# Kernel optimization log

Measured on AMD Instinct MI355X. Metric: run time of the kernel, lower is better.

The kernel has to match this reference:

```python
import jax, jax.numpy as jnp
import numpy as np

M, N, K, D_IN = 200, 6, 25, 784
GAMMA, EPS = 0.5, 0.5
TOTAL = M * N


def setup_inputs() -> dict:
    key = jax.random.key(0)
    ks = jax.random.split(key, 8)
    B = 16384
    def lin(kk, shape, fan_in):
        bound = 1.0 / np.sqrt(fan_in)
        return jax.random.uniform(kk, shape, jnp.float32, -bound, bound)
    return {
        "batch_x": jax.random.normal(ks[0], (B, D_IN), jnp.float32),
        "Wa": lin(ks[1], (M, D_IN), D_IN),
        "ba": lin(ks[2], (M,), D_IN),
        "Wb": lin(ks[3], (TOTAL, TOTAL), TOTAL),
        "bb": lin(ks[4], (TOTAL,), TOTAL),
        "Wd": lin(ks[5], (D_IN, M), M),
        "bd": lin(ks[6], (D_IN,), M),
    }


def _step(params, carry, x):
    Wa, ba, Wb, bb, Wd, bd = params
    x_b, phi, psi = carry
    # sigma: per-group drive broadcast over cells + full recurrent term, shape (m, n)
    z_a = (Wa @ x + ba)[:, None]                      # (m, 1)
    z_b = (Wb @ x_b + bb).reshape(M, N)               # (m, n)
    sigma = z_a + z_b
    # inhibited activity
    pi = (1.0 - phi) * (sigma - sigma.min() + 1.0)    # (m, n)
    lambda_i = pi.max(axis=1)                         # (m,)
    # top-1 cell per group (scatter of topk indices == one-hot argmax)
    M_pi = jax.nn.one_hot(jnp.argmax(pi, axis=1), N, dtype=sigma.dtype)
    # top-k groups
    _, idx = jax.lax.top_k(lambda_i, K)
    M_lambda = jnp.zeros((M,), sigma.dtype).at[idx].set(1.0)[:, None]
    y = jnp.tanh(M_pi * M_lambda * sigma)             # (m, n)
    x_a_pred = Wd @ y.max(axis=1) + bd                # (D_in,)
    # memory / inhibition updates
    psi_n = jnp.maximum(EPS * psi, y)
    phi_n = jnp.maximum(GAMMA * phi, y)
    alpha = psi_n.sum()
    alpha = jnp.where(alpha == 0.0, 1.0, alpha)
    x_b_n = (psi_n / alpha).reshape(-1)
    # original detaches the recurrent state each step
    carry_n = (jax.lax.stop_gradient(x_b_n),
               jax.lax.stop_gradient(phi_n),
               jax.lax.stop_gradient(psi_n))
    return carry_n, x_a_pred


def reference(batch_x, Wa, ba, Wb, bb, Wd, bd):
    params = (Wa, ba, Wb, bb, Wd, bd)
    carry0 = (jnp.zeros((TOTAL,), batch_x.dtype),
              jnp.zeros((M, N), batch_x.dtype),
              jnp.zeros((M, N), batch_x.dtype))
    (x_b, phi, psi), preds = jax.lax.scan(
        lambda c, x: _step(params, c, x), carry0, batch_x)
    return preds, x_b, phi, psi
```

## Files before the change

kernel.cpp:

```cpp
#include <hip/hip_runtime.h>
#include <math.h>

#define Tn   16384
#define Mg   200
#define Nc   6
#define TOT  1200
#define Kk   25
#define Din  784
#define PADG 8
#define CST  (Mg * PADG)

__global__ void transpose_k(const float* __restrict__ src, float* __restrict__ dst,
                            int R, int C) {
    __shared__ float tile[32][33];
    int bx = blockIdx.x * 32, by = blockIdx.y * 32;
    int x = bx + threadIdx.x;
    for (int j = 0; j < 32; j += 8) {
        int y = by + threadIdx.y + j;
        if (x < C && y < R) tile[threadIdx.y + j][threadIdx.x] = src[(size_t)y * C + x];
    }
    __syncthreads();
    int x2 = by + threadIdx.x;
    for (int j = 0; j < 32; j += 8) {
        int y2 = bx + threadIdx.y + j;
        if (x2 < R && y2 < C) dst[(size_t)y2 * R + x2] = tile[threadIdx.x][threadIdx.y + j];
    }
}

__global__ void wbT_pad_k(const float* __restrict__ Wb, float* __restrict__ WbTp) {
    __shared__ float tile[32][33];
    int e0 = blockIdx.x * 32, i0 = blockIdx.y * 32;
    for (int j = 0; j < 32; j += 8) {
        int i = i0 + threadIdx.y + j, e = e0 + threadIdx.x;
        if (i < TOT && e < TOT) tile[threadIdx.y + j][threadIdx.x] = Wb[(size_t)i * TOT + e];
    }
    __syncthreads();
    for (int j = 0; j < 32; j += 8) {
        int e = e0 + threadIdx.y + j, i = i0 + threadIdx.x;
        if (i < TOT && e < TOT) {
            int g = i / 6, c = i - 6 * g;
            WbTp[(size_t)e * CST + PADG * g + c] = tile[threadIdx.x][threadIdx.y + j];
        }
    }
}

__global__ void za_k(const float* __restrict__ X, const float* __restrict__ Wa,
                     const float* __restrict__ ba, float* __restrict__ Za) {
    __shared__ float xs[16][788];
    const int tid = threadIdx.x;
    const int t0  = blockIdx.x * 16;
    for (int idx = tid; idx < 16 * Din; idx += 256) {
        int tt = idx / Din, kk = idx - tt * Din;
        xs[tt][kk] = X[(size_t)(t0 + tt) * Din + kk];
    }
    __syncthreads();
    const int tq = tid & 15, gq = tid >> 4;
    const float4* xrow = reinterpret_cast<const float4*>(&xs[tq][0]);
    for (int g = gq; g < Mg; g += 16) {
        float acc = ba[g];
        const float4* wrow = reinterpret_cast<const float4*>(Wa + (size_t)g * Din);
        for (int k4 = 0; k4 < Din / 4; ++k4) {
            float4 a = xrow[k4], b = wrow[k4];
            acc = fmaf(a.x, b.x, acc); acc = fmaf(a.y, b.y, acc);
            acc = fmaf(a.z, b.z, acc); acc = fmaf(a.w, b.w, acc);
        }
        Za[(size_t)(t0 + tq) * Mg + g] = acc;
    }
}

__launch_bounds__(256, 1)
__global__ void serial_k(const float* __restrict__ Za, const float* __restrict__ WbTp,
                         const float* __restrict__ bb,
                         float* __restrict__ Yval, int* __restrict__ Yidx,
                         float* __restrict__ outTail) {
    __shared__ alignas(16) unsigned long long lamk[Mg];
    __shared__ alignas(16) unsigned long long sel[26];
    __shared__ alignas(16) float red[4];

    const int tid = threadIdx.x;
    const bool own = (tid < Mg);
    const int b = Nc * tid;

    float u0=0.f,u1=0.f,u2=0.f,u3=0.f,u4=0.f,u5=0.f;
    float p0=0.f,p1=0.f,p2=0.f,p3=0.f,p4=0.f,p5=0.f;
    float b0=0.f,b1=0.f,b2=0.f,b3=0.f,b4=0.f,b5=0.f;
    float alpha = 0.f;
    float zb = 0.f;
    if (own) {
        b0=bb[b]; b1=bb[b+1]; b2=bb[b+2]; b3=bb[b+3]; b4=bb[b+4]; b5=bb[b+5];
        zb = Za[tid];
    }
    if (tid == 255) sel[25] = 0ull;
    __syncthreads();

    const float* basep = WbTp + PADG * tid;

    for (int t = 0; t < Tn; ++t) {
        float inv = (alpha == 0.f) ? 1.f : (1.f / alpha);
        float s0=0,s1=0,s2=0,s3=0,s4=0,s5=0;
        float lmin = INFINITY;
        if (own) {
            float c = zb;
            s0 = fmaf(u0, inv, b0 + c); s1 = fmaf(u1, inv, b1 + c);
            s2 = fmaf(u2, inv, b2 + c); s3 = fmaf(u3, inv, b3 + c);
            s4 = fmaf(u4, inv, b4 + c); s5 = fmaf(u5, inv, b5 + c);
            lmin = fminf(fminf(fminf(s0,s1),fminf(s2,s3)),fminf(s4,s5));
        }
        for (int o = 32; o; o >>= 1) lmin = fminf(lmin, __shfl_down(lmin, o));
        if ((tid & 63) == 0) red[tid >> 6] = lmin;
        __syncthreads();

        float zn = 0.f;
        if (own && t + 1 < Tn) zn = Za[(size_t)(t + 1) * Mg + tid];

        unsigned long long myk = 0ull;
        float sb = 0.f, pb = 0.f;
        int bj = 0;
        if (own) {
            float4 r4 = *reinterpret_cast<const float4*>(red);
            float m1 = 1.f - fminf(fminf(r4.x, r4.y), fminf(r4.z, r4.w));
            float best = -INFINITY;
            float sa[6] = {s0,s1,s2,s3,s4,s5};
            float pa[6] = {p0,p1,p2,p3,p4,p5};
            #pragma unroll
            for (int j = 0; j < Nc; ++j) {
                float pv = (1.f - pa[j]) * (sa[j] + m1);
                if (pv > best) { best = pv; bj = j; sb = sa[j]; pb = pa[j]; }
            }
            unsigned int ub = __float_as_uint(best);
            ub ^= (unsigned int)(((int)ub) >> 31) | 0x80000000u;
            myk = ((unsigned long long)ub << 32) | (unsigned long long)(0xFFFFFFFFu - (unsigned)tid);
            lamk[tid] = myk;
        }
        __syncthreads();

        float d = 0.f;
        if (own) {
            float y  = tanhf(sb);
            float yv = fmaxf(y, 0.f);
            float dc = fmaxf(y - 0.5f * pb, 0.f);
            int r = 0;
            const ulonglong2* L = reinterpret_cast<const ulonglong2*>(lamk);
            #pragma unroll
            for (int q = 0; q < Mg / 2; ++q) {
                ulonglong2 kv = L[q];
                r += (kv.x > myk) + (kv.y > myk);
            }
            if (r < Kk) {
                d = dc;
                unsigned off = (unsigned)((b + bj) * CST);
                sel[r] = ((unsigned long long)off << 32) |
                         (unsigned long long)__float_as_uint(d);
                Yval[(size_t)t * Kk + r] = yv;
                Yidx[(size_t)t * Kk + r] = tid;
            }
            p0 = 0.5f*p0 + ((bj==0)?d:0.f); p1 = 0.5f*p1 + ((bj==1)?d:0.f);
            p2 = 0.5f*p2 + ((bj==2)?d:0.f); p3 = 0.5f*p3 + ((bj==3)?d:0.f);
            p4 = 0.5f*p4 + ((bj==4)?d:0.f); p5 = 0.5f*p5 + ((bj==5)?d:0.f);
        }
        __syncthreads();

        if (own) {
            ulonglong2 sraw[13];
            const ulonglong2* S = reinterpret_cast<const ulonglong2*>(sel);
            #pragma unroll
            for (int q = 0; q < 13; ++q) sraw[q] = S[q];
            float sd[Kk]; int so[Kk];
            #pragma unroll
            for (int k = 0; k < Kk; ++k) {
                unsigned long long v = (k & 1) ? sraw[k >> 1].y : sraw[k >> 1].x;
                sd[k] = __uint_as_float((unsigned)v);
                so[k] = (int)(v >> 32);
            }
            float asum = 0.f;
            #pragma unroll
            for (int k = 0; k < Kk; ++k) asum += sd[k];
            alpha = 0.5f * alpha + asum;

            float4 va[Kk]; float2 vb[Kk];
            #pragma unroll
            for (int k = 0; k < Kk; ++k) {
                const float* c = basep + so[k];
                va[k] = *reinterpret_cast<const float4*>(c);
                vb[k] = *reinterpret_cast<const float2*>(c + 4);
            }
            float a0=0.5f*u0, a1=0.5f*u1, a2=0.5f*u2, a3=0.5f*u3, a4=0.5f*u4, a5=0.5f*u5;
            #pragma unroll
            for (int k = 0; k < Kk; ++k) {
                float dk = sd[k];
                a0 = fmaf(dk, va[k].x, a0); a1 = fmaf(dk, va[k].y, a1);
                a2 = fmaf(dk, va[k].z, a2); a3 = fmaf(dk, va[k].w, a3);
                a4 = fmaf(dk, vb[k].x, a4); a5 = fmaf(dk, vb[k].y, a5);
            }
            u0=a0; u1=a1; u2=a2; u3=a3; u4=a4; u5=a5;
            zb = zn;
        }
    }

    if (own) {
        float inv = (alpha == 0.f) ? 1.f : (1.f / alpha);
        float pa[6] = {p0,p1,p2,p3,p4,p5};
        #pragma unroll
        for (int j = 0; j < Nc; ++j) {
            outTail[b + j]           = pa[j] * inv;
            outTail[TOT + b + j]     = pa[j];
            outTail[2 * TOT + b + j] = pa[j];
        }
    }
}

__global__ void preds_k(const float* __restrict__ Yval, const int* __restrict__ Yidx,
                        const float* __restrict__ WdT, const float* __restrict__ bd,
                        float* __restrict__ out) {
    const int t = blockIdx.x;
    __shared__ float sv[Kk];
    __shared__ int   si[Kk];
    if (threadIdx.x < Kk) {
        sv[threadIdx.x] = Yval[(size_t)t * Kk + threadIdx.x];
        si[threadIdx.x] = Yidx[(size_t)t * Kk + threadIdx.x];
    }
    __syncthreads();
    for (int d = threadIdx.x; d < Din; d += 256) {
        float acc = bd[d];
        #pragma unroll
        for (int k = 0; k < Kk; ++k)
            acc = fmaf(sv[k], WdT[(size_t)si[k] * Din + d], acc);
        out[(size_t)t * Din + d] = acc;
    }
}

extern "C" void kernel_launch(void* const* d_in, const int* in_sizes, int n_in,
                              void* d_out, int out_size, void* d_ws, size_t ws_size,
                              hipStream_t stream) {
    const float* X  = (const float*)d_in[0];
    const float* Wa = (const float*)d_in[1];
    const float* ba = (const float*)d_in[2];
    const float* Wb = (const float*)d_in[3];
    const float* bb = (const float*)d_in[4];
    const float* Wd = (const float*)d_in[5];
    const float* bd = (const float*)d_in[6];
    float* out = (float*)d_out;

    float* w    = (float*)d_ws;
    float* Za   = w;
    float* WbTp = Za   + (size_t)Tn * Mg;
    float* WdT  = WbTp + (size_t)TOT * CST;
    float* Yv   = WdT  + (size_t)Mg * Din;
    int*   Yi   = (int*)(Yv + (size_t)Tn * Kk);

    dim3 tb(32, 8);
    wbT_pad_k<<<dim3(38, 38), tb, 0, stream>>>(Wb, WbTp);
    transpose_k<<<dim3((Mg + 31) / 32, (Din + 31) / 32), tb, 0, stream>>>(Wd, WdT, Din, Mg);
    za_k<<<Tn / 16, 256, 0, stream>>>(X, Wa, ba, Za);
    serial_k<<<1, 256, 0, stream>>>(Za, WbTp, bb, Yv, Yi, out + (size_t)Tn * Din);
    preds_k<<<Tn, 256, 0, stream>>>(Yv, Yi, WdT, bd, out);
}
```

Measured before the change: 82.81 ms.

## Split serial recurrence across two thread halves with shared partial sums

Doubles the serial kernel to 512 threads. Each half computes part of the top-k rank count, and each half gathers about half of the 25 selected Wb columns. The second half's partial recurrent contribution goes through shared memory and is added at the start of the next step. The padded Wb transpose is replaced by a plain transpose read as float2 pairs, and an extra barrier per step is added. The aim is to shorten the per-step latency chain, at the cost of more synchronisation.

```diff
diff --git a/kernel.cpp b/kernel.cpp
--- a/kernel.cpp
+++ b/kernel.cpp
@@ -7,8 +7,6 @@
 #define TOT  1200
 #define Kk   25
 #define Din  784
-#define PADG 8
-#define CST  (Mg * PADG)
 
 __global__ void transpose_k(const float* __restrict__ src, float* __restrict__ dst,
                             int R, int C) {
@@ -24,23 +22,6 @@
     for (int j = 0; j < 32; j += 8) {
         int y2 = bx + threadIdx.y + j;
         if (x2 < R && y2 < C) dst[(size_t)y2 * R + x2] = tile[threadIdx.x][threadIdx.y + j];
-    }
-}
-
-__global__ void wbT_pad_k(const float* __restrict__ Wb, float* __restrict__ WbTp) {
-    __shared__ float tile[32][33];
-    int e0 = blockIdx.x * 32, i0 = blockIdx.y * 32;
-    for (int j = 0; j < 32; j += 8) {
-        int i = i0 + threadIdx.y + j, e = e0 + threadIdx.x;
-        if (i < TOT && e < TOT) tile[threadIdx.y + j][threadIdx.x] = Wb[(size_t)i * TOT + e];
-    }
-    __syncthreads();
-    for (int j = 0; j < 32; j += 8) {
-        int e = e0 + threadIdx.y + j, i = i0 + threadIdx.x;
-        if (i < TOT && e < TOT) {
-            int g = i / 6, c = i - 6 * g;
-            WbTp[(size_t)e * CST + PADG * g + c] = tile[threadIdx.x][threadIdx.y + j];
-        }
     }
 }
 
@@ -68,55 +49,62 @@
     }
 }
 
-__launch_bounds__(256, 1)
-__global__ void serial_k(const float* __restrict__ Za, const float* __restrict__ WbTp,
+__launch_bounds__(512, 1)
+__global__ void serial_k(const float* __restrict__ Za, const float* __restrict__ WbT,
                          const float* __restrict__ bb,
                          float* __restrict__ Yval, int* __restrict__ Yidx,
                          float* __restrict__ outTail) {
     __shared__ alignas(16) unsigned long long lamk[Mg];
     __shared__ alignas(16) unsigned long long sel[26];
     __shared__ alignas(16) float red[4];
+    __shared__ alignas(16) float uB[TOT];
+    __shared__ int rpart[Mg];
 
     const int tid = threadIdx.x;
-    const bool own = (tid < Mg);
-    const int b = Nc * tid;
+    const bool Aside = (tid < 256);
+    const int g = Aside ? tid : tid - 256;
+    const bool own  = (g < Mg);
+    const bool ownA = Aside && own;
+    const int b = Nc * g;
 
     float u0=0.f,u1=0.f,u2=0.f,u3=0.f,u4=0.f,u5=0.f;
     float p0=0.f,p1=0.f,p2=0.f,p3=0.f,p4=0.f,p5=0.f;
     float b0=0.f,b1=0.f,b2=0.f,b3=0.f,b4=0.f,b5=0.f;
-    float alpha = 0.f;
-    float zb = 0.f;
-    if (own) {
+    float alpha = 0.f, zb = 0.f;
+    if (ownA) {
         b0=bb[b]; b1=bb[b+1]; b2=bb[b+2]; b3=bb[b+3]; b4=bb[b+4]; b5=bb[b+5];
-        zb = Za[tid];
-    }
-    if (tid == 255) sel[25] = 0ull;
-    __syncthreads();
-
-    const float* basep = WbTp + PADG * tid;
+        zb = Za[g];
+    }
+    for (int i = tid; i < TOT; i += 512) uB[i] = 0.f;
+    __syncthreads();
+
+    const float* baseW = WbT + b;
 
     for (int t = 0; t < Tn; ++t) {
-        float inv = (alpha == 0.f) ? 1.f : (1.f / alpha);
+        float zn = 0.f;
+        if (ownA && t + 1 < Tn) zn = Za[(size_t)(t + 1) * Mg + g];
+
+        unsigned long long myk = 0ull;
+        float sb=0.f, pb=0.f; int bj = 0;
+        float lmin = INFINITY;
         float s0=0,s1=0,s2=0,s3=0,s4=0,s5=0;
-        float lmin = INFINITY;
-        if (own) {
-            float c = zb;
-            s0 = fmaf(u0, inv, b0 + c); s1 = fmaf(u1, inv, b1 + c);
-            s2 = fmaf(u2, inv, b2 + c); s3 = fmaf(u3, inv, b3 + c);
-            s4 = fmaf(u4, inv, b4 + c); s5 = fmaf(u5, inv, b5 + c);
+        if (ownA) {
+            const float2* q = reinterpret_cast<const float2*>(&uB[b]);
+            float2 q0=q[0], q1=q[1], q2=q[2];
+            u0+=q0.x; u1+=q0.y; u2+=q1.x; u3+=q1.y; u4+=q2.x; u5+=q2.y;
+            float inv = (alpha == 0.f) ? 1.f : (1.f / alpha);
+            s0 = fmaf(u0, inv, b0 + zb); s1 = fmaf(u1, inv, b1 + zb);
+            s2 = fmaf(u2, inv, b2 + zb); s3 = fmaf(u3, inv, b3 + zb);
+            s4 = fmaf(u4, inv, b4 + zb); s5 = fmaf(u5, inv, b5 + zb);
             lmin = fminf(fminf(fminf(s0,s1),fminf(s2,s3)),fminf(s4,s5));
         }
-        for (int o = 32; o; o >>= 1) lmin = fminf(lmin, __shfl_down(lmin, o));
-        if ((tid & 63) == 0) red[tid >> 6] = lmin;
-        __syncthreads();
-
-        float zn = 0.f;
-        if (own && t + 1 < Tn) zn = Za[(size_t)(t + 1) * Mg + tid];
-
-        unsigned long long myk = 0ull;
-        float sb = 0.f, pb = 0.f;
-        int bj = 0;
-        if (own) {
+        if (Aside) {
+            for (int o = 32; o; o >>= 1) lmin = fminf(lmin, __shfl_down(lmin, o));
+            if ((tid & 63) == 0) red[tid >> 6] = lmin;
+        }
+        __syncthreads();
+
+        if (ownA) {
             float4 r4 = *reinterpret_cast<const float4*>(red);
             float m1 = 1.f - fminf(fminf(r4.x, r4.y), fminf(r4.z, r4.w));
             float best = -INFINITY;
@@ -127,32 +115,36 @@
                 float pv = (1.f - pa[j]) * (sa[j] + m1);
                 if (pv > best) { best = pv; bj = j; sb = sa[j]; pb = pa[j]; }
             }
-            unsigned int ub = __float_as_uint(best);
-            ub ^= (unsigned int)(((int)ub) >> 31) | 0x80000000u;
-            myk = ((unsigned long long)ub << 32) | (unsigned long long)(0xFFFFFFFFu - (unsigned)tid);
-            lamk[tid] = myk;
-        }
-        __syncthreads();
-
-        float d = 0.f;
+            unsigned ub = __float_as_uint(best);
+            ub ^= (unsigned)(((int)ub) >> 31) | 0x80000000u;
+            myk = ((unsigned long long)ub << 32) | (unsigned long long)(0xFFFFFFFFu - (unsigned)g);
+            lamk[g] = myk;
+        }
+        __syncthreads();
+
+        int rr = 0; float yv = 0.f, dc = 0.f;
         if (own) {
-            float y  = tanhf(sb);
-            float yv = fmaxf(y, 0.f);
-            float dc = fmaxf(y - 0.5f * pb, 0.f);
-            int r = 0;
-            const ulonglong2* L = reinterpret_cast<const ulonglong2*>(lamk);
-            #pragma unroll
-            for (int q = 0; q < Mg / 2; ++q) {
+            if (!Aside) myk = lamk[g];
+            const ulonglong2* L = reinterpret_cast<const ulonglong2*>(lamk) + (Aside ? 0 : 50);
+            #pragma unroll
+            for (int q = 0; q < 50; ++q) {
                 ulonglong2 kv = L[q];
-                r += (kv.x > myk) + (kv.y > myk);
-            }
+                rr += (kv.x > myk) + (kv.y > myk);
+            }
+            if (ownA) { float y = tanhf(sb); yv = fmaxf(y, 0.f); dc = fmaxf(y - 0.5f * pb, 0.f); }
+        }
+        if (!Aside && own) rpart[g] = rr;
+        __syncthreads();
+
+        if (ownA) {
+            int r = rr + rpart[g];
+            float d = 0.f;
             if (r < Kk) {
                 d = dc;
-                unsigned off = (unsigned)((b + bj) * CST);
-                sel[r] = ((unsigned long long)off << 32) |
+                sel[r] = ((unsigned long long)(unsigned)((b + bj) * TOT) << 32) |
                          (unsigned long long)__float_as_uint(d);
                 Yval[(size_t)t * Kk + r] = yv;
-                Yidx[(size_t)t * Kk + r] = tid;
+                Yidx[(size_t)t * Kk + r] = g;
             }
             p0 = 0.5f*p0 + ((bj==0)?d:0.f); p1 = 0.5f*p1 + ((bj==1)?d:0.f);
             p2 = 0.5f*p2 + ((bj==2)?d:0.f); p3 = 0.5f*p3 + ((bj==3)?d:0.f);
@@ -172,32 +164,58 @@
                 sd[k] = __uint_as_float((unsigned)v);
                 so[k] = (int)(v >> 32);
             }
-            float asum = 0.f;
-            #pragma unroll
-            for (int k = 0; k < Kk; ++k) asum += sd[k];
-            alpha = 0.5f * alpha + asum;
-
-            float4 va[Kk]; float2 vb[Kk];
-            #pragma unroll
-            for (int k = 0; k < Kk; ++k) {
-                const float* c = basep + so[k];
-                va[k] = *reinterpret_cast<const float4*>(c);
-                vb[k] = *reinterpret_cast<const float2*>(c + 4);
-            }
-            float a0=0.5f*u0, a1=0.5f*u1, a2=0.5f*u2, a3=0.5f*u3, a4=0.5f*u4, a5=0.5f*u5;
-            #pragma unroll
-            for (int k = 0; k < Kk; ++k) {
-                float dk = sd[k];
-                a0 = fmaf(dk, va[k].x, a0); a1 = fmaf(dk, va[k].y, a1);
-                a2 = fmaf(dk, va[k].z, a2); a3 = fmaf(dk, va[k].w, a3);
-                a4 = fmaf(dk, vb[k].x, a4); a5 = fmaf(dk, vb[k].y, a5);
-            }
-            u0=a0; u1=a1; u2=a2; u3=a3; u4=a4; u5=a5;
-            zb = zn;
-        }
-    }
-
-    if (own) {
+            if (Aside) {
+                float asum = 0.f;
+                #pragma unroll
+                for (int k = 0; k < Kk; ++k) asum += sd[k];
+                alpha = 0.5f * alpha + asum;
+                float2 c0[13], c1[13], c2[13];
+                #pragma unroll
+                for (int k = 0; k < 13; ++k) {
+                    const float* cp = baseW + so[k];
+                    c0[k] = *reinterpret_cast<const float2*>(cp);
+                    c1[k] = *reinterpret_cast<const float2*>(cp + 2);
+                    c2[k] = *reinterpret_cast<const float2*>(cp + 4);
+                }
+                __builtin_amdgcn_sched_barrier(0);
+                float a0=0.5f*u0, a1=0.5f*u1, a2=0.5f*u2, a3=0.5f*u3, a4=0.5f*u4, a5=0.5f*u5;
+                #pragma unroll
+                for (int k = 0; k < 13; ++k) {
+                    float dk = sd[k];
+                    a0 = fmaf(dk, c0[k].x, a0); a1 = fmaf(dk, c0[k].y, a1);
+                    a2 = fmaf(dk, c1[k].x, a2); a3 = fmaf(dk, c1[k].y, a3);
+                    a4 = fmaf(dk, c2[k].x, a4); a5 = fmaf(dk, c2[k].y, a5);
+                }
+                u0=a0; u1=a1; u2=a2; u3=a3; u4=a4; u5=a5;
+                zb = zn;
+            } else {
+                float2 c0[12], c1[12], c2[12];
+                #pragma unroll
+                for (int k = 0; k < 12; ++k) {
+                    const float* cp = baseW + so[13 + k];
+                    c0[k] = *reinterpret_cast<const float2*>(cp);
+                    c1[k] = *reinterpret_cast<const float2*>(cp + 2);
+                    c2[k] = *reinterpret_cast<const float2*>(cp + 4);
+                }
+                __builtin_amdgcn_sched_barrier(0);
+                float a0=0,a1=0,a2=0,a3=0,a4=0,a5=0;
+                #pragma unroll
+                for (int k = 0; k < 12; ++k) {
+                    float dk = sd[13 + k];
+                    a0 = fmaf(dk, c0[k].x, a0); a1 = fmaf(dk, c0[k].y, a1);
+                    a2 = fmaf(dk, c1[k].x, a2); a3 = fmaf(dk, c1[k].y, a3);
+                    a4 = fmaf(dk, c2[k].x, a4); a5 = fmaf(dk, c2[k].y, a5);
+                }
+                float2* w = reinterpret_cast<float2*>(&uB[b]);
+                w[0] = make_float2(a0, a1);
+                w[1] = make_float2(a2, a3);
+                w[2] = make_float2(a4, a5);
+            }
+        }
+        __syncthreads();
+    }
+
+    if (ownA) {
         float inv = (alpha == 0.f) ? 1.f : (1.f / alpha);
         float pa[6] = {p0,p1,p2,p3,p4,p5};
         #pragma unroll
@@ -243,15 +261,15 @@
 
     float* w    = (float*)d_ws;
     float* Za   = w;
-    float* WbTp = Za   + (size_t)Tn * Mg;
-    float* WdT  = WbTp + (size_t)TOT * CST;
-    float* Yv   = WdT  + (size_t)Mg * Din;
+    float* WbT  = Za  + (size_t)Tn * Mg;
+    float* WdT  = WbT + (size_t)TOT * TOT;
+    float* Yv   = WdT + (size_t)Mg * Din;
     int*   Yi   = (int*)(Yv + (size_t)Tn * Kk);
 
     dim3 tb(32, 8);
-    wbT_pad_k<<<dim3(38, 38), tb, 0, stream>>>(Wb, WbTp);
+    transpose_k<<<dim3((TOT + 31) / 32, (TOT + 31) / 32), tb, 0, stream>>>(Wb, WbT, TOT, TOT);
     transpose_k<<<dim3((Mg + 31) / 32, (Din + 31) / 32), tb, 0, stream>>>(Wd, WdT, Din, Mg);
     za_k<<<Tn / 16, 256, 0, stream>>>(X, Wa, ba, Za);
-    serial_k<<<1, 256, 0, stream>>>(Za, WbTp, bb, Yv, Yi, out + (size_t)Tn * Din);
+    serial_k<<<1, 512, 0, stream>>>(Za, WbT, bb, Yv, Yi, out + (size_t)Tn * Din);
     preds_k<<<Tn, 256, 0, stream>>>(Yv, Yi, WdT, bd, out);
 }
```

Result: slower. 85.88 ms (+3.7%).

## Stage Za chunks in LDS and batch top-k outputs in serial kernel

Applied to the files above, without the earlier changes.

The serial kernel now copies 32 timesteps of Za into shared memory at a time instead of doing a per-step global load. It also buffers the packed (index, value) top-k outputs in LDS and writes them out once per chunk as 64-bit words. The Wb layout drops the padded 8-stride in favour of a plain transpose, so each gathered column now takes three float2 loads instead of a float4 plus a float2. A sched_barrier separates the loads from the FMAs. This is meant to take global-memory latency off the serial critical path, at the cost of a block sync every 32 steps and more LDS use.

```diff
diff --git a/kernel.cpp b/kernel.cpp
--- a/kernel.cpp
+++ b/kernel.cpp
@@ -7,8 +7,7 @@
 #define TOT  1200
 #define Kk   25
 #define Din  784
-#define PADG 8
-#define CST  (Mg * PADG)
+#define CH   32
 
 __global__ void transpose_k(const float* __restrict__ src, float* __restrict__ dst,
                             int R, int C) {
@@ -24,23 +23,6 @@
     for (int j = 0; j < 32; j += 8) {
         int y2 = bx + threadIdx.y + j;
         if (x2 < R && y2 < C) dst[(size_t)y2 * R + x2] = tile[threadIdx.x][threadIdx.y + j];
-    }
-}
-
-__global__ void wbT_pad_k(const float* __restrict__ Wb, float* __restrict__ WbTp) {
-    __shared__ float tile[32][33];
-    int e0 = blockIdx.x * 32, i0 = blockIdx.y * 32;
-    for (int j = 0; j < 32; j += 8) {
-        int i = i0 + threadIdx.y + j, e = e0 + threadIdx.x;
-        if (i < TOT && e < TOT) tile[threadIdx.y + j][threadIdx.x] = Wb[(size_t)i * TOT + e];
-    }
-    __syncthreads();
-    for (int j = 0; j < 32; j += 8) {
-        int e = e0 + threadIdx.y + j, i = i0 + threadIdx.x;
-        if (i < TOT && e < TOT) {
-            int g = i / 6, c = i - 6 * g;
-            WbTp[(size_t)e * CST + PADG * g + c] = tile[threadIdx.x][threadIdx.y + j];
-        }
     }
 }
 
@@ -69,13 +51,15 @@
 }
 
 __launch_bounds__(256, 1)
-__global__ void serial_k(const float* __restrict__ Za, const float* __restrict__ WbTp,
+__global__ void serial_k(const float* __restrict__ Za, const float* __restrict__ WbT,
                          const float* __restrict__ bb,
-                         float* __restrict__ Yval, int* __restrict__ Yidx,
+                         unsigned long long* __restrict__ YP,
                          float* __restrict__ outTail) {
     __shared__ alignas(16) unsigned long long lamk[Mg];
     __shared__ alignas(16) unsigned long long sel[26];
     __shared__ alignas(16) float red[4];
+    __shared__ alignas(16) float zs[CH * Mg];
+    __shared__ alignas(16) unsigned long long ypk[CH * Kk];
 
     const int tid = threadIdx.x;
     const bool own = (tid < Mg);
@@ -85,37 +69,40 @@
     float p0=0.f,p1=0.f,p2=0.f,p3=0.f,p4=0.f,p5=0.f;
     float b0=0.f,b1=0.f,b2=0.f,b3=0.f,b4=0.f,b5=0.f;
     float alpha = 0.f;
-    float zb = 0.f;
     if (own) {
         b0=bb[b]; b1=bb[b+1]; b2=bb[b+2]; b3=bb[b+3]; b4=bb[b+4]; b5=bb[b+5];
-        zb = Za[tid];
-    }
-    if (tid == 255) sel[25] = 0ull;
-    __syncthreads();
-
-    const float* basep = WbTp + PADG * tid;
+    }
+    #pragma unroll
+    for (int i = 0; i < 7; ++i) {
+        int idx = i * 1024 + tid * 4;
+        if (idx < CH * Mg) {
+            float4 v = *reinterpret_cast<const float4*>(Za + idx);
+            *reinterpret_cast<float4*>(zs + idx) = v;
+        }
+    }
+    __syncthreads();
+
+    const float* baseW = WbT + b;
 
     for (int t = 0; t < Tn; ++t) {
-        float inv = (alpha == 0.f) ? 1.f : (1.f / alpha);
+        const int tc = t & (CH - 1);
+
         float s0=0,s1=0,s2=0,s3=0,s4=0,s5=0;
         float lmin = INFINITY;
         if (own) {
-            float c = zb;
-            s0 = fmaf(u0, inv, b0 + c); s1 = fmaf(u1, inv, b1 + c);
-            s2 = fmaf(u2, inv, b2 + c); s3 = fmaf(u3, inv, b3 + c);
-            s4 = fmaf(u4, inv, b4 + c); s5 = fmaf(u5, inv, b5 + c);
+            float zbv = zs[tc * Mg + tid];
+            float inv = (alpha == 0.f) ? 1.f : (1.f / alpha);
+            s0 = fmaf(u0, inv, b0 + zbv); s1 = fmaf(u1, inv, b1 + zbv);
+            s2 = fmaf(u2, inv, b2 + zbv); s3 = fmaf(u3, inv, b3 + zbv);
+            s4 = fmaf(u4, inv, b4 + zbv); s5 = fmaf(u5, inv, b5 + zbv);
             lmin = fminf(fminf(fminf(s0,s1),fminf(s2,s3)),fminf(s4,s5));
         }
         for (int o = 32; o; o >>= 1) lmin = fminf(lmin, __shfl_down(lmin, o));
         if ((tid & 63) == 0) red[tid >> 6] = lmin;
         __syncthreads();
 
-        float zn = 0.f;
-        if (own && t + 1 < Tn) zn = Za[(size_t)(t + 1) * Mg + tid];
-
         unsigned long long myk = 0ull;
-        float sb = 0.f, pb = 0.f;
-        int bj = 0;
+        float sb=0.f, pb=0.f; int bj = 0;
         if (own) {
             float4 r4 = *reinterpret_cast<const float4*>(red);
             float m1 = 1.f - fminf(fminf(r4.x, r4.y), fminf(r4.z, r4.w));
@@ -127,14 +114,13 @@
                 float pv = (1.f - pa[j]) * (sa[j] + m1);
                 if (pv > best) { best = pv; bj = j; sb = sa[j]; pb = pa[j]; }
             }
-            unsigned int ub = __float_as_uint(best);
-            ub ^= (unsigned int)(((int)ub) >> 31) | 0x80000000u;
+            unsigned ub = __float_as_uint(best);
+            ub ^= (unsigned)(((int)ub) >> 31) | 0x80000000u;
             myk = ((unsigned long long)ub << 32) | (unsigned long long)(0xFFFFFFFFu - (unsigned)tid);
             lamk[tid] = myk;
         }
         __syncthreads();
 
-        float d = 0.f;
         if (own) {
             float y  = tanhf(sb);
             float yv = fmaxf(y, 0.f);
@@ -142,17 +128,17 @@
             int r = 0;
             const ulonglong2* L = reinterpret_cast<const ulonglong2*>(lamk);
             #pragma unroll
-            for (int q = 0; q < Mg / 2; ++q) {
-                ulonglong2 kv = L[q];
+            for (int qq = 0; qq < Mg / 2; ++qq) {
+                ulonglong2 kv = L[qq];
                 r += (kv.x > myk) + (kv.y > myk);
             }
+            float d = 0.f;
             if (r < Kk) {
                 d = dc;
-                unsigned off = (unsigned)((b + bj) * CST);
-                sel[r] = ((unsigned long long)off << 32) |
+                sel[r] = ((unsigned long long)(unsigned)((b + bj) * TOT) << 32) |
                          (unsigned long long)__float_as_uint(d);
-                Yval[(size_t)t * Kk + r] = yv;
-                Yidx[(size_t)t * Kk + r] = tid;
+                ypk[tc * Kk + r] = ((unsigned long long)(unsigned)tid << 32) |
+                                   (unsigned long long)__float_as_uint(yv);
             }
             p0 = 0.5f*p0 + ((bj==0)?d:0.f); p1 = 0.5f*p1 + ((bj==1)?d:0.f);
             p2 = 0.5f*p2 + ((bj==2)?d:0.f); p3 = 0.5f*p3 + ((bj==3)?d:0.f);
@@ -164,7 +150,7 @@
             ulonglong2 sraw[13];
             const ulonglong2* S = reinterpret_cast<const ulonglong2*>(sel);
             #pragma unroll
-            for (int q = 0; q < 13; ++q) sraw[q] = S[q];
+            for (int qq = 0; qq < 13; ++qq) sraw[qq] = S[qq];
             float sd[Kk]; int so[Kk];
             #pragma unroll
             for (int k = 0; k < Kk; ++k) {
@@ -177,23 +163,42 @@
             for (int k = 0; k < Kk; ++k) asum += sd[k];
             alpha = 0.5f * alpha + asum;
 
-            float4 va[Kk]; float2 vb[Kk];
+            float2 c0[Kk], c1[Kk], c2[Kk];
             #pragma unroll
             for (int k = 0; k < Kk; ++k) {
-                const float* c = basep + so[k];
-                va[k] = *reinterpret_cast<const float4*>(c);
-                vb[k] = *reinterpret_cast<const float2*>(c + 4);
-            }
+                const float* cp = baseW + so[k];
+                c0[k] = *reinterpret_cast<const float2*>(cp);
+                c1[k] = *reinterpret_cast<const float2*>(cp + 2);
+                c2[k] = *reinterpret_cast<const float2*>(cp + 4);
+            }
+            __builtin_amdgcn_sched_barrier(0);
             float a0=0.5f*u0, a1=0.5f*u1, a2=0.5f*u2, a3=0.5f*u3, a4=0.5f*u4, a5=0.5f*u5;
             #pragma unroll
             for (int k = 0; k < Kk; ++k) {
                 float dk = sd[k];
-                a0 = fmaf(dk, va[k].x, a0); a1 = fmaf(dk, va[k].y, a1);
-                a2 = fmaf(dk, va[k].z, a2); a3 = fmaf(dk, va[k].w, a3);
-                a4 = fmaf(dk, vb[k].x, a4); a5 = fmaf(dk, vb[k].y, a5);
+                a0 = fmaf(dk, c0[k].x, a0); a1 = fmaf(dk, c0[k].y, a1);
+                a2 = fmaf(dk, c1[k].x, a2); a3 = fmaf(dk, c1[k].y, a3);
+                a4 = fmaf(dk, c2[k].x, a4); a5 = fmaf(dk, c2[k].y, a5);
             }
             u0=a0; u1=a1; u2=a2; u3=a3; u4=a4; u5=a5;
-            zb = zn;
+        }
+
+        if (tc == CH - 1) {
+            const size_t t0 = (size_t)(t - (CH - 1)) * Kk;
+            for (int i = tid; i < CH * Kk; i += 256)
+                YP[t0 + i] = ypk[i];
+            if (t + 1 < Tn) {
+                const float* src = Za + (size_t)(t + 1) * Mg;
+                #pragma unroll
+                for (int i = 0; i < 7; ++i) {
+                    int idx = i * 1024 + tid * 4;
+                    if (idx < CH * Mg) {
+                        float4 v = *reinterpret_cast<const float4*>(src + idx);
+                        *reinterpret_cast<float4*>(zs + idx) = v;
+                    }
+                }
+            }
+            __syncthreads();
         }
     }
 
@@ -209,15 +214,16 @@
     }
 }
 
-__global__ void preds_k(const float* __restrict__ Yval, const int* __restrict__ Yidx,
+__global__ void preds_k(const unsigned long long* __restrict__ YP,
                         const float* __restrict__ WdT, const float* __restrict__ bd,
                         float* __restrict__ out) {
     const int t = blockIdx.x;
     __shared__ float sv[Kk];
     __shared__ int   si[Kk];
     if (threadIdx.x < Kk) {
-        sv[threadIdx.x] = Yval[(size_t)t * Kk + threadIdx.x];
-        si[threadIdx.x] = Yidx[(size_t)t * Kk + threadIdx.x];
+        unsigned long long v = YP[(size_t)t * Kk + threadIdx.x];
+        sv[threadIdx.x] = __uint_as_float((unsigned)v);
+        si[threadIdx.x] = (int)(v >> 32);
     }
     __syncthreads();
     for (int d = threadIdx.x; d < Din; d += 256) {
@@ -243,15 +249,15 @@
 
     float* w    = (float*)d_ws;
     float* Za   = w;
-    float* WbTp = Za   + (size_t)Tn * Mg;
-    float* WdT  = WbTp + (size_t)TOT * CST;
-    float* Yv   = WdT  + (size_t)Mg * Din;
-    int*   Yi   = (int*)(Yv + (size_t)Tn * Kk);
+    float* WbT  = Za  + (size_t)Tn * Mg;
+    float* WdT  = WbT + (size_t)TOT * TOT;
+    unsigned long long* YP =
+        (unsigned long long*)(WdT + (size_t)Mg * Din);
 
     dim3 tb(32, 8);
-    wbT_pad_k<<<dim3(38, 38), tb, 0, stream>>>(Wb, WbTp);
+    transpose_k<<<dim3((TOT + 31) / 32, (TOT + 31) / 32), tb, 0, stream>>>(Wb, WbT, TOT, TOT);
     transpose_k<<<dim3((Mg + 31) / 32, (Din + 31) / 32), tb, 0, stream>>>(Wd, WdT, Din, Mg);
     za_k<<<Tn / 16, 256, 0, stream>>>(X, Wa, ba, Za);
-    serial_k<<<1, 256, 0, stream>>>(Za, WbTp, bb, Yv, Yi, out + (size_t)Tn * Din);
-    preds_k<<<Tn, 256, 0, stream>>>(Yv, Yi, WdT, bd, out);
-}
+    serial_k<<<1, 256, 0, stream>>>(Za, WbT, bb, YP, out + (size_t)Tn * Din);
+    preds_k<<<Tn, 256, 0, stream>>>(YP, WdT, bd, out);
+}
```

Result: faster. 78.09 ms (-5.7%).
